# Kernel tuning notes

Measured on AMD Instinct MI355X. Metric: run time of the kernel, lower is better.

Reference implementation:

```python
import jax, jax.numpy as jnp
import numpy as np

BETA = 0.25  # commitment_cost; use_ema=True path -> vq_loss = beta * mse(z_e, sg(z_q))


def setup_inputs() -> dict:
    key = jax.random.key(0)
    k1, k2 = jax.random.split(key)
    B, T, K, D = 8192, 16, 512, 128
    z_e = jax.random.normal(k1, (B, T, D), dtype=jnp.float32)
    # matches nn.init.uniform_(cb.weight, -1/K, 1/K), stacked over T slots
    codebooks = jax.random.uniform(k2, (T, K, D), dtype=jnp.float32,
                                   minval=-1.0 / K, maxval=1.0 / K)
    return {"z_e": z_e, "codebooks": codebooks}


def reference(z_e, codebooks):
    # z_e: (B, T, D); codebooks: (T, K, D)
    B, T, D = z_e.shape
    K = codebooks.shape[1]
    # per-slot squared distances: ||z||^2 - 2 z.w + ||w||^2 -> (B, T, K)
    distances = (jnp.sum(z_e * z_e, axis=-1, keepdims=True)
                 - 2.0 * jnp.einsum('btd,tkd->btk', z_e, codebooks)
                 + jnp.sum(codebooks * codebooks, axis=-1)[None, :, :])
    tokens = jnp.argmin(distances, axis=-1)          # (B, T) int
    # gather per-slot code vectors
    z_q = codebooks[jnp.arange(T)[None, :], tokens]  # (B, T, D)
    # straight-through estimator
    z_q_st = z_e + jax.lax.stop_gradient(z_q - z_e)
    # sum_t beta*mse_t / T == beta * mean over all elements (each slot mse is a B*D mean)
    vq_loss = BETA * jnp.mean(jnp.square(z_e - jax.lax.stop_gradient(z_q)))
    # utilization: total unique codes used per slot / (T*K)
    used = jnp.zeros((T, K), dtype=bool).at[jnp.arange(T)[None, :], tokens].set(True)
    utilization = jnp.sum(used).astype(jnp.float32) / (T * K)
    return z_q_st, tokens, vq_loss, utilization
```

## Files before the change

kernel.cpp:

```cpp
#include <hip/hip_runtime.h>
#include <cfloat>

#define TT 16
#define KK 512
#define DD 128
#define BSTRIPE 512
#define BC 32
#define NW 8
#define NCHUNK (BSTRIPE / BC)
#define N0 16777216
#define N1 131072
#define TAU 1e-4f

typedef _Float16 half8 __attribute__((ext_vector_type(8)));
typedef float f32x16 __attribute__((ext_vector_type(16)));

__device__ __forceinline__ float np_sum128_sq_f4(const float4* __restrict__ p) {
  float4 a = p[0], b = p[1];
  float r[8];
  r[0] = __fmul_rn(a.x, a.x); r[1] = __fmul_rn(a.y, a.y);
  r[2] = __fmul_rn(a.z, a.z); r[3] = __fmul_rn(a.w, a.w);
  r[4] = __fmul_rn(b.x, b.x); r[5] = __fmul_rn(b.y, b.y);
  r[6] = __fmul_rn(b.z, b.z); r[7] = __fmul_rn(b.w, b.w);
#pragma unroll
  for (int i = 1; i < 16; ++i) {
    a = p[2 * i]; b = p[2 * i + 1];
    r[0] = __fadd_rn(r[0], __fmul_rn(a.x, a.x));
    r[1] = __fadd_rn(r[1], __fmul_rn(a.y, a.y));
    r[2] = __fadd_rn(r[2], __fmul_rn(a.z, a.z));
    r[3] = __fadd_rn(r[3], __fmul_rn(a.w, a.w));
    r[4] = __fadd_rn(r[4], __fmul_rn(b.x, b.x));
    r[5] = __fadd_rn(r[5], __fmul_rn(b.y, b.y));
    r[6] = __fadd_rn(r[6], __fmul_rn(b.z, b.z));
    r[7] = __fadd_rn(r[7], __fmul_rn(b.w, b.w));
  }
  return __fadd_rn(__fadd_rn(__fadd_rn(r[0], r[1]), __fadd_rn(r[2], r[3])),
                   __fadd_rn(__fadd_rn(r[4], r[5]), __fadd_rn(r[6], r[7])));
}

__device__ __forceinline__ float dot128_chain(const float* __restrict__ zp,
                                              const float* __restrict__ cp) {
  float s = 0.0f;
#pragma unroll
  for (int d4 = 0; d4 < 32; ++d4) {
    const float4 a = *(const float4*)(zp + d4 * 4);
    const float4 c = *(const float4*)(cp + d4 * 4);
    s = __builtin_fmaf(a.x, c.x, s);
    s = __builtin_fmaf(a.y, c.y, s);
    s = __builtin_fmaf(a.z, c.z, s);
    s = __builtin_fmaf(a.w, c.w, s);
  }
  return s;
}

__device__ __forceinline__ void split8(const float4 a, const float4 b, const float sc,
                                       half8& h1, half8& h2) {
  const float v[8] = {a.x, a.y, a.z, a.w, b.x, b.y, b.z, b.w};
#pragma unroll
  for (int i = 0; i < 8; ++i) {
    const float s = __fmul_rn(v[i], sc);
    const _Float16 p = (_Float16)s;
    const float rr = __fsub_rn(s, (float)p);
    h1[i] = p;
    h2[i] = (_Float16)rr;
  }
}

__device__ __forceinline__ half8 split8_hi(const float4 a, const float4 b, const float sc) {
  const float v[8] = {a.x, a.y, a.z, a.w, b.x, b.y, b.z, b.w};
  half8 h;
#pragma unroll
  for (int i = 0; i < 8; ++i) h[i] = (_Float16)__fmul_rn(v[i], sc);
  return h;
}

__global__ void __launch_bounds__(512, 1)
vq_main(const float* __restrict__ z_e, const float* __restrict__ cb,
        float* __restrict__ out, float* __restrict__ loss_part,
        int* __restrict__ used) {
  __shared__ alignas(16) _Float16 cb2s[KK * DD];
  __shared__ alignas(16) _Float16 zs[BC * 256];
  __shared__ float qs[KK];
  __shared__ float As[BC];
  __shared__ int tok_s[BC];
  __shared__ unsigned long long mrg[BC * NW * 2];
  __shared__ float wred[NW];

  const int tid = threadIdx.x;
  const int t = blockIdx.y;
  const int bbase = blockIdx.x * BSTRIPE;
  const int w = tid >> 6;
  const int lane = tid & 63;
  const int lr = lane & 31;
  const int lhi = lane >> 5;

  {
    const int k = tid;
    const float* src = cb + ((size_t)t * KK + k) * DD;
    float r[8];
    half8 p1, p2;
    {
      const float4 a = *(const float4*)(src);
      const float4 b = *(const float4*)(src + 4);
      r[0] = __fmul_rn(a.x, a.x); r[1] = __fmul_rn(a.y, a.y);
      r[2] = __fmul_rn(a.z, a.z); r[3] = __fmul_rn(a.w, a.w);
      r[4] = __fmul_rn(b.x, b.x); r[5] = __fmul_rn(b.y, b.y);
      r[6] = __fmul_rn(b.z, b.z); r[7] = __fmul_rn(b.w, b.w);
      split8(a, b, 8192.0f, p1, p2);
      *(half8*)(cb2s + k * DD + ((0 ^ (k & 15)) * 8)) = p2;
    }
#pragma unroll
    for (int g = 1; g < 16; ++g) {
      const float4 a = *(const float4*)(src + g * 8);
      const float4 b = *(const float4*)(src + g * 8 + 4);
      r[0] = __fadd_rn(r[0], __fmul_rn(a.x, a.x));
      r[1] = __fadd_rn(r[1], __fmul_rn(a.y, a.y));
      r[2] = __fadd_rn(r[2], __fmul_rn(a.z, a.z));
      r[3] = __fadd_rn(r[3], __fmul_rn(a.w, a.w));
      r[4] = __fadd_rn(r[4], __fmul_rn(b.x, b.x));
      r[5] = __fadd_rn(r[5], __fmul_rn(b.y, b.y));
      r[6] = __fadd_rn(r[6], __fmul_rn(b.z, b.z));
      r[7] = __fadd_rn(r[7], __fmul_rn(b.w, b.w));
      split8(a, b, 8192.0f, p1, p2);
      *(half8*)(cb2s + k * DD + ((g ^ (k & 15)) * 8)) = p2;
    }
    qs[k] = __fadd_rn(__fadd_rn(__fadd_rn(r[0], r[1]), __fadd_rn(r[2], r[3])),
                      __fadd_rn(__fadd_rn(r[4], r[5]), __fadd_rn(r[6], r[7])));
  }

  half8 ca[2][8];
#pragma unroll
  for (int mt = 0; mt < 2; ++mt) {
    const int krow = w * 64 + mt * 32 + lr;
    const float* src = cb + ((size_t)t * KK + krow) * DD + 8 * lhi;
#pragma unroll
    for (int ds = 0; ds < 8; ++ds) {
      const float4 a = *(const float4*)(src + ds * 16);
      const float4 b = *(const float4*)(src + ds * 16 + 4);
      ca[mt][ds] = split8_hi(a, b, 8192.0f);
    }
  }

  float lsum = 0.0f;
  const int srow = tid >> 4, sunit = tid & 15;

  float4 pza, pzb;
  {
    const float* zp = z_e + ((size_t)(bbase + srow) * TT + t) * DD + sunit * 8;
    pza = *(const float4*)zp;
    pzb = *(const float4*)(zp + 4);
  }

#pragma unroll 1
  for (int bc = 0; bc < NCHUNK; ++bc) {
    const int b0 = bbase + bc * BC;
    __syncthreads();

    {
      half8 p1, p2;
      split8(pza, pzb, 128.0f, p1, p2);
      const int c1 = sunit ^ srow;
      const int c2 = (16 + sunit) ^ srow;
      *(half8*)(zs + srow * 256 + c1 * 8) = p1;
      *(half8*)(zs + srow * 256 + c2 * 8) = p2;
      if (tid < BC)
        As[tid] = np_sum128_sq_f4(
            (const float4*)(z_e + ((size_t)(b0 + tid) * TT + t) * DD));
    }
    __syncthreads();

    if (bc + 1 < NCHUNK) {
      const float* zp =
          z_e + ((size_t)(b0 + BC + srow) * TT + t) * DD + sunit * 8;
      pza = *(const float4*)zp;
      pzb = *(const float4*)(zp + 4);
    }

    f32x16 acc0, acc1;
#pragma unroll
    for (int i = 0; i < 16; ++i) { acc0[i] = 0.0f; acc1[i] = 0.0f; }

#pragma unroll
    for (int ds = 0; ds < 8; ++ds) {
      const int ch = (ds * 2 + lhi) ^ lr;
      const half8 bf = *(const half8*)(zs + lr * 256 + ch * 8);
      acc0 = __builtin_amdgcn_mfma_f32_32x32x16_f16(ca[0][ds], bf, acc0, 0, 0, 0);
      acc1 = __builtin_amdgcn_mfma_f32_32x32x16_f16(ca[1][ds], bf, acc1, 0, 0, 0);
    }
#pragma unroll
    for (int ds = 0; ds < 8; ++ds) {
      const int g = ds * 2 + lhi;
      const int ch = g ^ lr;
      const half8 bf = *(const half8*)(zs + lr * 256 + ch * 8);
      const half8 a2_0 =
          *(const half8*)(cb2s + (size_t)(w * 64 + lr) * DD + ((g ^ (lr & 15)) * 8));
      const half8 a2_1 =
          *(const half8*)(cb2s + (size_t)(w * 64 + 32 + lr) * DD + ((g ^ (lr & 15)) * 8));
      acc0 = __builtin_amdgcn_mfma_f32_32x32x16_f16(a2_0, bf, acc0, 0, 0, 0);
      acc1 = __builtin_amdgcn_mfma_f32_32x32x16_f16(a2_1, bf, acc1, 0, 0, 0);
    }
#pragma unroll
    for (int ds = 0; ds < 8; ++ds) {
      const int ch = (16 + ds * 2 + lhi) ^ lr;
      const half8 bf2 = *(const half8*)(zs + lr * 256 + ch * 8);
      acc0 = __builtin_amdgcn_mfma_f32_32x32x16_f16(ca[0][ds], bf2, acc0, 0, 0, 0);
      acc1 = __builtin_amdgcn_mfma_f32_32x32x16_f16(ca[1][ds], bf2, acc1, 0, 0, 0);
    }

    const float Ab = As[lr];
    unsigned long long b1 = ~0ULL, b2 = ~0ULL;
#pragma unroll
    for (int mt = 0; mt < 2; ++mt) {
#pragma unroll
      for (int r = 0; r < 16; ++r) {
        const int k = w * 64 + mt * 32 + (r & 3) + 8 * (r >> 2) + 4 * lhi;
        const float av = (mt == 0) ? acc0[r] : acc1[r];
        const float dist =
            __fadd_rn(__fsub_rn(Ab, __fmul_rn(av, 0x1p-19f)), qs[k]);
        const unsigned long long cand =
            ((unsigned long long)__float_as_uint(dist) << 32) | (unsigned)k;
        if (cand < b1) { b2 = b1; b1 = cand; }
        else if (cand < b2) { b2 = cand; }
      }
    }
    {
      const unsigned long long o1 = __shfl_xor(b1, 32, 64);
      const unsigned long long o2 = __shfl_xor(b2, 32, 64);
      const unsigned long long lo = (b1 < o1) ? b1 : o1;
      const unsigned long long hi = (b1 < o1) ? o1 : b1;
      const unsigned long long s2 = (b2 < o2) ? b2 : o2;
      b1 = lo;
      b2 = (hi < s2) ? hi : s2;
    }
    if (lane < 32) {
      mrg[lr * (NW * 2) + w * 2] = b1;
      mrg[lr * (NW * 2) + w * 2 + 1] = b2;
    }
    __syncthreads();

    if (tid < BC) {
      unsigned long long m1 = ~0ULL, m2 = ~0ULL;
#pragma unroll
      for (int g = 0; g < NW * 2; ++g) {
        const unsigned long long v = mrg[tid * (NW * 2) + g];
        if (v < m1) { m2 = m1; m1 = v; }
        else if (v < m2) { m2 = v; }
      }
      int tok = (int)(m1 & 0xffffffffULL);
      const float d1 = __uint_as_float((unsigned)(m1 >> 32));
      const float d2 = __uint_as_float((unsigned)(m2 >> 32));
      if (d2 - d1 < TAU) {
        const int k1 = (int)(m1 & 0xffffffffULL);
        const int k2 = (int)(m2 & 0xffffffffULL);
        const float* zp = z_e + ((size_t)(b0 + tid) * TT + t) * DD;
        const float Az = As[tid];
        const float e1 = dot128_chain(zp, cb + ((size_t)t * KK + k1) * DD);
        const float e2 = dot128_chain(zp, cb + ((size_t)t * KK + k2) * DD);
        const float dd1 = __fadd_rn(__fsub_rn(Az, __fmul_rn(2.0f, e1)), qs[k1]);
        const float dd2 = __fadd_rn(__fsub_rn(Az, __fmul_rn(2.0f, e2)), qs[k2]);
        const unsigned long long c1 =
            ((unsigned long long)__float_as_uint(dd1) << 32) | (unsigned)k1;
        const unsigned long long c2 =
            ((unsigned long long)__float_as_uint(dd2) << 32) | (unsigned)k2;
        tok = (int)(((c1 < c2) ? c1 : c2) & 0xffffffffULL);
      }
      tok_s[tid] = tok;
      out[(size_t)N0 + (size_t)(b0 + tid) * TT + t] = (float)tok;
      atomicOr(&used[t * KK + tok], 1);
    }
    __syncthreads();

    {
      const int k = tok_s[srow];
      const float* zp = z_e + ((size_t)(b0 + srow) * TT + t) * DD + sunit * 8;
      const float* cp = cb + ((size_t)t * KK + k) * DD + sunit * 8;
      float* op = out + ((size_t)(b0 + srow) * TT + t) * DD + sunit * 8;
#pragma unroll
      for (int h = 0; h < 2; ++h) {
        const float4 zv = *(const float4*)(zp + h * 4);
        const float4 cv = *(const float4*)(cp + h * 4);
        float4 o;
        o.x = __fadd_rn(zv.x, __fsub_rn(cv.x, zv.x));
        o.y = __fadd_rn(zv.y, __fsub_rn(cv.y, zv.y));
        o.z = __fadd_rn(zv.z, __fsub_rn(cv.z, zv.z));
        o.w = __fadd_rn(zv.w, __fsub_rn(cv.w, zv.w));
        *(float4*)(op + h * 4) = o;
        const float dx = zv.x - cv.x, dy = zv.y - cv.y;
        const float dz = zv.z - cv.z, dw = zv.w - cv.w;
        lsum += dx * dx + dy * dy + dz * dz + dw * dw;
      }
    }
  }

#pragma unroll
  for (int off = 32; off > 0; off >>= 1) lsum += __shfl_down(lsum, off, 64);
  if (lane == 0) wred[w] = lsum;
  __syncthreads();
  if (tid == 0) {
    float s = 0.0f;
#pragma unroll
    for (int i = 0; i < NW; ++i) s += wred[i];
    loss_part[blockIdx.y * 16 + blockIdx.x] = s;
  }
}

__global__ void vq_final(const float* __restrict__ loss_part,
                         const int* __restrict__ used, float* __restrict__ out) {
  __shared__ float partf[4];
  __shared__ int   parti[4];
  int tid = threadIdx.x;
  float ls = 0.0f;
  for (int i = tid; i < 256; i += 256) ls += loss_part[i];
  int c = 0;
  for (int i = tid; i < TT * KK; i += 256) c += used[i];
#pragma unroll
  for (int off = 32; off > 0; off >>= 1) {
    ls += __shfl_down(ls, off, 64);
    c  += __shfl_down(c, off, 64);
  }
  if ((tid & 63) == 0) { partf[tid >> 6] = ls; parti[tid >> 6] = c; }
  __syncthreads();
  if (tid == 0) {
    float lt = partf[0] + partf[1] + partf[2] + partf[3];
    int   tot = parti[0] + parti[1] + parti[2] + parti[3];
    out[(size_t)N0 + N1]     = 0.25f * lt / 16777216.0f;
    out[(size_t)N0 + N1 + 1] = (float)tot / 8192.0f;
  }
}

extern "C" void kernel_launch(void* const* d_in, const int* in_sizes, int n_in,
                              void* d_out, int out_size, void* d_ws, size_t ws_size,
                              hipStream_t stream) {
  const float* z_e = (const float*)d_in[0];
  const float* cb  = (const float*)d_in[1];
  float* out = (float*)d_out;
  float* loss_part = (float*)d_ws;
  int*   used      = (int*)((char*)d_ws + 4096);
  hipMemsetAsync(d_ws, 0, 4096 + TT * KK * sizeof(int), stream);
  vq_main<<<dim3(8192 / BSTRIPE, TT), 512, 0, stream>>>(z_e, cb, out, loss_part, used);
  vq_final<<<1, 256, 0, stream>>>(loss_part, used, out);
}
```

Baseline: 307.8 us.

## Defer straight-through output to stripe end and parallelize token merge

The per-chunk squared-norm computation moves to a single pass over the whole 512-row stripe before the main loop. The per-chunk output writing (z_q_st, tokens, utilization atomics, loss) moves to one batched epilogue after all chunks, which removes one barrier per chunk and the serialized tail in which only 32 threads worked. The top-2 merge is now spread across warps (one thread per 16) and uses a transposed mrg layout. In exchange, z_e and codebook rows are re-read in a large burst at the end, so there is no overlap of that traffic with MFMA work, and shared memory for per-stripe arrays grows slightly.

Result: faster. 281.3 us (-8.6%).

```diff
diff --git a/kernel.cpp b/kernel.cpp
--- a/kernel.cpp
+++ b/kernel.cpp
@@ -81,9 +81,9 @@
   __shared__ alignas(16) _Float16 cb2s[KK * DD];
   __shared__ alignas(16) _Float16 zs[BC * 256];
   __shared__ float qs[KK];
-  __shared__ float As[BC];
-  __shared__ int tok_s[BC];
-  __shared__ unsigned long long mrg[BC * NW * 2];
+  __shared__ float As_all[BSTRIPE];
+  __shared__ int tok_all[BSTRIPE];
+  __shared__ unsigned long long mrg[(2 * NW) * BC];
   __shared__ float wred[NW];
 
   const int tid = threadIdx.x;
@@ -126,6 +126,8 @@
     }
     qs[k] = __fadd_rn(__fadd_rn(__fadd_rn(r[0], r[1]), __fadd_rn(r[2], r[3])),
                       __fadd_rn(__fadd_rn(r[4], r[5]), __fadd_rn(r[6], r[7])));
+    As_all[tid] = np_sum128_sq_f4(
+        (const float4*)(z_e + ((size_t)(bbase + tid) * TT + t) * DD));
   }
 
   half8 ca[2][8];
@@ -141,7 +143,6 @@
     }
   }
 
-  float lsum = 0.0f;
   const int srow = tid >> 4, sunit = tid & 15;
 
   float4 pza, pzb;
@@ -150,11 +151,11 @@
     pza = *(const float4*)zp;
     pzb = *(const float4*)(zp + 4);
   }
+  __syncthreads();
 
 #pragma unroll 1
   for (int bc = 0; bc < NCHUNK; ++bc) {
     const int b0 = bbase + bc * BC;
-    __syncthreads();
 
     {
       half8 p1, p2;
@@ -163,9 +164,6 @@
       const int c2 = (16 + sunit) ^ srow;
       *(half8*)(zs + srow * 256 + c1 * 8) = p1;
       *(half8*)(zs + srow * 256 + c2 * 8) = p2;
-      if (tid < BC)
-        As[tid] = np_sum128_sq_f4(
-            (const float4*)(z_e + ((size_t)(b0 + tid) * TT + t) * DD));
     }
     __syncthreads();
 
@@ -207,7 +205,7 @@
       acc1 = __builtin_amdgcn_mfma_f32_32x32x16_f16(ca[1][ds], bf2, acc1, 0, 0, 0);
     }
 
-    const float Ab = As[lr];
+    const float Ab = As_all[bc * BC + lr];
     unsigned long long b1 = ~0ULL, b2 = ~0ULL;
 #pragma unroll
     for (int mt = 0; mt < 2; ++mt) {
@@ -233,27 +231,28 @@
       b2 = (hi < s2) ? hi : s2;
     }
     if (lane < 32) {
-      mrg[lr * (NW * 2) + w * 2] = b1;
-      mrg[lr * (NW * 2) + w * 2 + 1] = b2;
+      mrg[(w * 2) * BC + lr] = b1;
+      mrg[(w * 2 + 1) * BC + lr] = b2;
     }
     __syncthreads();
 
-    if (tid < BC) {
+    if ((tid & 15) == 0) {
+      const int row = tid >> 4;
       unsigned long long m1 = ~0ULL, m2 = ~0ULL;
 #pragma unroll
-      for (int g = 0; g < NW * 2; ++g) {
-        const unsigned long long v = mrg[tid * (NW * 2) + g];
+      for (int g = 0; g < 2 * NW; ++g) {
+        const unsigned long long v = mrg[g * BC + row];
         if (v < m1) { m2 = m1; m1 = v; }
         else if (v < m2) { m2 = v; }
       }
       int tok = (int)(m1 & 0xffffffffULL);
-      const float d1 = __uint_as_float((unsigned)(m1 >> 32));
-      const float d2 = __uint_as_float((unsigned)(m2 >> 32));
-      if (d2 - d1 < TAU) {
+      const float d1f = __uint_as_float((unsigned)(m1 >> 32));
+      const float d2f = __uint_as_float((unsigned)(m2 >> 32));
+      if (d2f - d1f < TAU) {
         const int k1 = (int)(m1 & 0xffffffffULL);
         const int k2 = (int)(m2 & 0xffffffffULL);
-        const float* zp = z_e + ((size_t)(b0 + tid) * TT + t) * DD;
-        const float Az = As[tid];
+        const float* zp = z_e + ((size_t)(b0 + row) * TT + t) * DD;
+        const float Az = As_all[bc * BC + row];
         const float e1 = dot128_chain(zp, cb + ((size_t)t * KK + k1) * DD);
         const float e2 = dot128_chain(zp, cb + ((size_t)t * KK + k2) * DD);
         const float dd1 = __fadd_rn(__fsub_rn(Az, __fmul_rn(2.0f, e1)), qs[k1]);
@@ -264,31 +263,38 @@
             ((unsigned long long)__float_as_uint(dd2) << 32) | (unsigned)k2;
         tok = (int)(((c1 < c2) ? c1 : c2) & 0xffffffffULL);
       }
-      tok_s[tid] = tok;
-      out[(size_t)N0 + (size_t)(b0 + tid) * TT + t] = (float)tok;
-      atomicOr(&used[t * KK + tok], 1);
-    }
-    __syncthreads();
-
-    {
-      const int k = tok_s[srow];
-      const float* zp = z_e + ((size_t)(b0 + srow) * TT + t) * DD + sunit * 8;
-      const float* cp = cb + ((size_t)t * KK + k) * DD + sunit * 8;
-      float* op = out + ((size_t)(b0 + srow) * TT + t) * DD + sunit * 8;
-#pragma unroll
-      for (int h = 0; h < 2; ++h) {
-        const float4 zv = *(const float4*)(zp + h * 4);
-        const float4 cv = *(const float4*)(cp + h * 4);
-        float4 o;
-        o.x = __fadd_rn(zv.x, __fsub_rn(cv.x, zv.x));
-        o.y = __fadd_rn(zv.y, __fsub_rn(cv.y, zv.y));
-        o.z = __fadd_rn(zv.z, __fsub_rn(cv.z, zv.z));
-        o.w = __fadd_rn(zv.w, __fsub_rn(cv.w, zv.w));
-        *(float4*)(op + h * 4) = o;
-        const float dx = zv.x - cv.x, dy = zv.y - cv.y;
-        const float dz = zv.z - cv.z, dw = zv.w - cv.w;
-        lsum += dx * dx + dy * dy + dz * dz + dw * dw;
-      }
+      tok_all[bc * BC + row] = tok;
+    }
+  }
+  __syncthreads();
+
+  {
+    const int tok = tok_all[tid];
+    out[(size_t)N0 + (size_t)(bbase + tid) * TT + t] = (float)tok;
+    atomicOr(&used[t * KK + tok], 1);
+  }
+  float lsum = 0.0f;
+#pragma unroll
+  for (int it = 0; it < 16; ++it) {
+    const int idx = tid + it * 512;
+    const int row = idx >> 4, unit = idx & 15;
+    const int k = tok_all[row];
+    const float* zp = z_e + ((size_t)(bbase + row) * TT + t) * DD + unit * 8;
+    const float* cp = cb + ((size_t)t * KK + k) * DD + unit * 8;
+    float* op = out + ((size_t)(bbase + row) * TT + t) * DD + unit * 8;
+#pragma unroll
+    for (int h = 0; h < 2; ++h) {
+      const float4 zv = *(const float4*)(zp + h * 4);
+      const float4 cv = *(const float4*)(cp + h * 4);
+      float4 o;
+      o.x = __fadd_rn(zv.x, __fsub_rn(cv.x, zv.x));
+      o.y = __fadd_rn(zv.y, __fsub_rn(cv.y, zv.y));
+      o.z = __fadd_rn(zv.z, __fsub_rn(cv.z, zv.z));
+      o.w = __fadd_rn(zv.w, __fsub_rn(cv.w, zv.w));
+      *(float4*)(op + h * 4) = o;
+      const float dx = zv.x - cv.x, dy = zv.y - cv.y;
+      const float dz = zv.z - cv.z, dw = zv.w - cv.w;
+      lsum += dx * dx + dy * dy + dz * dz + dw * dw;
     }
   }
 
```
